# Kernel optimization log

Hardware: AMD Instinct MI355X
Metric: run time of the kernel (lower is better)

The kernel has to match this reference:

```python
import jax, jax.numpy as jnp
import numpy as np

B, S, E, H = 4, 1024, 512, 8
DK = E // H


def setup_inputs() -> dict:
    key = jax.random.key(0)
    ks = jax.random.split(key, 16)
    s = 1.0 / np.sqrt(E)
    inp = {
        "query": jax.random.normal(ks[0], (B, S, E), dtype=jnp.float32),
        "key": jax.random.normal(ks[1], (B, S, E), dtype=jnp.float32),
        "value": jax.random.normal(ks[2], (B, S, E), dtype=jnp.float32),
        "dist_conv": jax.random.uniform(ks[3], (B, S, S), dtype=jnp.float32),
        "mask": jax.random.randint(ks[4], (B, S, S), 0, 2, dtype=jnp.int32),
        # four Linear(E, E) layers: q, k, v, out (torch: y = x @ W.T + b)
        "Wq": jax.random.normal(ks[5], (E, E), dtype=jnp.float32) * s,
        "bq": jnp.zeros((E,), dtype=jnp.float32),
        "Wk": jax.random.normal(ks[6], (E, E), dtype=jnp.float32) * s,
        "bk": jnp.zeros((E,), dtype=jnp.float32),
        "Wv": jax.random.normal(ks[7], (E, E), dtype=jnp.float32) * s,
        "bv": jnp.zeros((E,), dtype=jnp.float32),
        "Wo": jax.random.normal(ks[8], (E, E), dtype=jnp.float32) * s,
        "bo": jnp.zeros((E,), dtype=jnp.float32),
        # 1x1 Conv2d(1, H) -> ReLU -> 1x1 Conv2d(H, H)
        "cw1": jax.random.normal(ks[9], (H,), dtype=jnp.float32),  # [out_c] (in_c=1, k=1)
        "cb1": jnp.zeros((H,), dtype=jnp.float32),
        "cw2": jax.random.normal(ks[10], (H, H), dtype=jnp.float32) * (1.0 / np.sqrt(H)),
        "cb2": jnp.zeros((H,), dtype=jnp.float32),
    }
    return inp


def reference(query, key, value, dist_conv, mask, Wq, bq, Wk, bk, Wv, bv, Wo, bo, cw1, cb1, cw2, cb2):
    # projections, split into heads: [B, H, S, DK]
    def proj(x, W, b):
        y = jnp.einsum("bse,fe->bsf", x, W) + b
        return y.reshape(B, S, H, DK).transpose(0, 2, 1, 3)

    q = proj(query, Wq, bq)
    k = proj(key, Wk, bk)
    v = proj(value, Wv, bv)

    # 1x1 conv stack on distance matrix: [B,S,S] -> [B,H,S,S]
    t = jax.nn.relu(dist_conv[:, None] * cw1[None, :, None, None] + cb1[None, :, None, None])
    bias = jnp.einsum("bhij,gh->bgij", t, cw2) + cb2[None, :, None, None]

    scores = jnp.einsum("bhqd,bhkd->bhqk", q, k) / jnp.sqrt(jnp.float32(DK))
    scores = scores * bias
    scores = jnp.where(mask[:, None] == 0, jnp.float32(-1e9), scores)
    p_attn = jax.nn.softmax(scores, axis=-1)

    x = jnp.einsum("bhqk,bhkd->bhqd", p_attn, v)
    x = x.transpose(0, 2, 1, 3).reshape(B, S, E)
    return jnp.einsum("bse,fe->bsf", x, Wo) + bo
```

## Files before the change

### kernel.cpp

```cpp
#include <hip/hip_runtime.h>
#include <hip/hip_bf16.h>
#include <math.h>

#define B_ 4
#define S_ 1024
#define E_ 512
#define H_ 8
#define DK_ 64

typedef short bf16x8 __attribute__((ext_vector_type(8)));
typedef float f32x4 __attribute__((ext_vector_type(4)));

#define MFMA16(a, b, c) __builtin_amdgcn_mfma_f32_16x16x32_bf16((a), (b), (c), 0, 0, 0)
#define cfence() asm volatile("" ::: "memory")

__device__ __forceinline__ void gl_lds16(const void* gptr, void* lptr) {
    __builtin_amdgcn_global_load_lds(
        (const __attribute__((address_space(1))) unsigned int*)gptr,
        (__attribute__((address_space(3))) unsigned int*)lptr,
        16, 0, 0);
}

__device__ __forceinline__ unsigned short bf16_bits(float v) {
    __hip_bfloat16 h = __float2bfloat16(v);
    return *(unsigned short*)&h;
}

__global__ __launch_bounds__(256) void prep(
    const float* __restrict__ q, const float* __restrict__ k, const float* __restrict__ v,
    const float* __restrict__ wq, const float* __restrict__ wk,
    const float* __restrict__ wv, const float* __restrict__ wo,
    const float* __restrict__ dist, const int* __restrict__ mask,
    const float* __restrict__ cw1, const float* __restrict__ cb1,
    const float* __restrict__ cw2, const float* __restrict__ cb2,
    __hip_bfloat16* qc, __hip_bfloat16* kc, __hip_bfloat16* vc,
    __hip_bfloat16* wqc, __hip_bfloat16* wkc, __hip_bfloat16* wvc, __hip_bfloat16* woc,
    __hip_bfloat16* __restrict__ biasS) {
    const int blk = blockIdx.x;
    if (blk >= 3584) {
        const int bi = blk - 3584;
        const int b = bi >> 10, i = bi & 1023;
        const int j0 = threadIdx.x * 4;
        const size_t dbase = ((size_t)b * 1024 + i) * 1024 + j0;
        float4 d4 = *(const float4*)(dist + dbase);
        int4 m4 = *(const int4*)(mask + dbase);
        float dv[4] = {d4.x, d4.y, d4.z, d4.w};
        int mv[4] = {m4.x, m4.y, m4.z, m4.w};
        float tt[4][8];
#pragma unroll
        for (int e = 0; e < 4; ++e)
#pragma unroll
            for (int h = 0; h < 8; ++h)
                tt[e][h] = fmaxf(fmaf(dv[e], cw1[h], cb1[h]), 0.f);
#pragma unroll
        for (int g = 0; g < 8; ++g) {
            const float c2 = cb2[g];
            union { unsigned short us[4]; uint2 u2; } o;
#pragma unroll
            for (int e = 0; e < 4; ++e) {
                float bv = c2;
#pragma unroll
                for (int h = 0; h < 8; ++h) bv = fmaf(tt[e][h], cw2[g * 8 + h], bv);
                unsigned short u = bf16_bits(bv * 0.125f);
                if (mv[e] == 0) u = 0xFF80u;
                o.us[e] = u;
            }
            *(uint2*)(biasS + ((size_t)(b * 8 + g) * 1024 + i) * 1024 + j0) = o.u2;
        }
        return;
    }
    const float* src;
    __hip_bfloat16* dst;
    int base;
    if (blk < 1024)      { src = q; dst = qc; base = blk; }
    else if (blk < 2048) { src = k; dst = kc; base = blk - 1024; }
    else if (blk < 3072) { src = v; dst = vc; base = blk - 2048; }
    else {
        const int wz = (blk - 3072) >> 7;
        base = (blk - 3072) & 127;
        switch (wz) {
            case 0: src = wq; dst = wqc; break;
            case 1: src = wk; dst = wkc; break;
            case 2: src = wv; dst = wvc; break;
            default: src = wo; dst = woc; break;
        }
    }
    const int idx = (base * 256 + threadIdx.x) * 8;
    float4 a = *(const float4*)(src + idx);
    float4 bb = *(const float4*)(src + idx + 4);
    union { __hip_bfloat16 h[8]; uint4 u; } o;
    o.h[0] = __float2bfloat16(a.x);  o.h[1] = __float2bfloat16(a.y);
    o.h[2] = __float2bfloat16(a.z);  o.h[3] = __float2bfloat16(a.w);
    o.h[4] = __float2bfloat16(bb.x); o.h[5] = __float2bfloat16(bb.y);
    o.h[6] = __float2bfloat16(bb.z); o.h[7] = __float2bfloat16(bb.w);
    *(uint4*)(dst + idx) = o.u;
}

template <int NROWS_W, int NT>
__device__ __forceinline__ void gemm_core128(const __hip_bfloat16* A, const __hip_bfloat16* W,
                                             char* sA, char* sW, int m0, int n0,
                                             f32x4 acc[4][NT]) {
    const int t = threadIdx.x;
    const int w = t >> 6, lane = t & 63;
    const int wm = (w >> 1) * 64, wn = (w & 1) * (NT * 16);
    const int g = lane >> 4, ln = lane & 15;

    for (int kc = 0; kc < 4; ++kc) {
        __syncthreads();
#pragma unroll
        for (int i = 0; i < 8; ++i) {
            int L = (i * 4 + w) * 64 + lane;
            int r = L >> 4, cs = L & 15;
            int c = cs ^ (r & 15);
            gl_lds16((const char*)A + (size_t)(m0 + r) * 1024 + kc * 256 + c * 16,
                     sA + (i * 4 + w) * 1024);
        }
#pragma unroll
        for (int i = 0; i < NROWS_W / 16; ++i) {
            int L = (i * 4 + w) * 64 + lane;
            int r = L >> 4, cs = L & 15;
            int c = cs ^ (r & 15);
            gl_lds16((const char*)W + (size_t)(n0 + r) * 1024 + kc * 256 + c * 16,
                     sW + (i * 4 + w) * 1024);
        }
        __syncthreads();
#pragma unroll
        for (int ks = 0; ks < 4; ++ks) {
            bf16x8 af[4], bf[NT];
#pragma unroll
            for (int mt = 0; mt < 4; ++mt) {
                int m = wm + mt * 16 + ln;
                int c = ks * 4 + g;
                af[mt] = *(const bf16x8*)(sA + m * 256 + (c ^ (m & 15)) * 16);
            }
#pragma unroll
            for (int nt = 0; nt < NT; ++nt) {
                int n = wn + nt * 16 + ln;
                int c = ks * 4 + g;
                bf[nt] = *(const bf16x8*)(sW + n * 256 + (c ^ (n & 15)) * 16);
            }
#pragma unroll
            for (int mt = 0; mt < 4; ++mt)
#pragma unroll
                for (int nt = 0; nt < NT; ++nt)
                    acc[mt][nt] = MFMA16(af[mt], bf[nt], acc[mt][nt]);
        }
    }
}

__global__ __launch_bounds__(256) void proj_gemm(
    const __hip_bfloat16* __restrict__ qc, const __hip_bfloat16* __restrict__ kc,
    const __hip_bfloat16* __restrict__ vc,
    const __hip_bfloat16* __restrict__ wqc, const __hip_bfloat16* __restrict__ wkc,
    const __hip_bfloat16* __restrict__ wvc,
    const float* __restrict__ bq, const float* __restrict__ bk, const float* __restrict__ bv,
    __hip_bfloat16* qbh, __hip_bfloat16* kbh, __hip_bfloat16* vt) {
    __shared__ char smem[65536];
    char* sA = smem;
    char* sW = smem + 32768;
    const int z = blockIdx.z;
    const __hip_bfloat16* A;
    const __hip_bfloat16* W;
    const float* bias;
    __hip_bfloat16* dst;
    if (z == 0)      { A = qc; W = wqc; bias = bq; dst = qbh; }
    else if (z == 1) { A = kc; W = wkc; bias = bk; dst = kbh; }
    else             { A = vc; W = wvc; bias = bv; dst = vt; }

    const int m0 = blockIdx.y * 128, n0 = blockIdx.x * 128;
    f32x4 acc[4][4] = {};
    gemm_core128<128, 4>(A, W, sA, sW, m0, n0, acc);
    __syncthreads();

    const int t = threadIdx.x;
    const int w = t >> 6, lane = t & 63;
    const int wm = (w >> 1) * 64, wn = (w & 1) * 64;
    const int g = lane >> 4, ln = lane & 15;
    const int b = m0 >> 10;
    float bv4[4];
#pragma unroll
    for (int nt = 0; nt < 4; ++nt) bv4[nt] = bias[n0 + wn + nt * 16 + ln];

    __hip_bfloat16* T = (__hip_bfloat16*)smem;
    if (z != 2) {
#pragma unroll
        for (int p = 0; p < 2; ++p) {
            if (wm == p * 64) {
#pragma unroll
                for (int mt = 0; mt < 4; ++mt)
#pragma unroll
                    for (int nt = 0; nt < 4; ++nt)
#pragma unroll
                        for (int r = 0; r < 4; ++r)
                            T[(mt * 16 + g * 4 + r) * 136 + wn + nt * 16 + ln] =
                                __float2bfloat16(acc[mt][nt][r] + bv4[nt]);
            }
            __syncthreads();
            const int lr = t >> 2, quarter = t & 3;
            const char* srow = (const char*)T + lr * 272 + quarter * 64;
            const int s = (m0 & 1023) + p * 64 + lr;
            const int h = (n0 >> 6) + (quarter >> 1);
            char* gdst = (char*)dst +
                         (((size_t)(b * 8 + h) * 1024 + s) * 64 + (quarter & 1) * 32) * 2;
#pragma unroll
            for (int j = 0; j < 4; ++j)
                *(uint4*)(gdst + j * 16) = *(const uint4*)(srow + j * 16);
            __syncthreads();
        }
    } else {
#pragma unroll
        for (int p = 0; p < 2; ++p) {
            if (wm == p * 64) {
#pragma unroll
                for (int mt = 0; mt < 4; ++mt)
#pragma unroll
                    for (int nt = 0; nt < 4; ++nt)
#pragma unroll
                        for (int r = 0; r < 4; ++r)
                            T[(mt * 16 + g * 4 + r) * 130 + wn + nt * 16 + ln] =
                                __float2bfloat16(acc[mt][nt][r] + bv4[nt]);
            }
            __syncthreads();
            const int c = t >> 1, sel = t & 1;
            union { __hip_bfloat16 h[32]; uint4 u[4]; } P;
#pragma unroll
            for (int i = 0; i < 32; ++i)
                P.h[i] = T[(sel * 32 + i) * 130 + c];
            const int h = (n0 >> 6) + (c >> 6), dk = c & 63;
            char* gdst = (char*)vt +
                         (((size_t)(b * 8 + h) * 64 + dk) * 1024 + (m0 & 1023) + p * 64 + sel * 32) * 2;
#pragma unroll
            for (int j = 0; j < 4; ++j)
                *(uint4*)(gdst + j * 16) = P.u[j];
            __syncthreads();
        }
    }
}

__global__ __launch_bounds__(256) void out_gemm(
    const __hip_bfloat16* __restrict__ X, const __hip_bfloat16* __restrict__ woc,
    const float* __restrict__ bo, float* __restrict__ out) {
    __shared__ char smem[49152];
    char* sA = smem;
    char* sW = smem + 32768;
    const int m0 = blockIdx.y * 128, n0 = blockIdx.x * 64;
    f32x4 acc[4][2] = {};
    gemm_core128<64, 2>(X, woc, sA, sW, m0, n0, acc);

    const int t = threadIdx.x;
    const int w = t >> 6, lane = t & 63;
    const int wm = (w >> 1) * 64, wn = (w & 1) * 32;
    const int g = lane >> 4, ln = lane & 15;
    float bv2[2];
#pragma unroll
    for (int nt = 0; nt < 2; ++nt) bv2[nt] = bo[n0 + wn + nt * 16 + ln];
#pragma unroll
    for (int mt = 0; mt < 4; ++mt)
#pragma unroll
        for (int nt = 0; nt < 2; ++nt)
#pragma unroll
            for (int r = 0; r < 4; ++r) {
                int m = m0 + wm + mt * 16 + g * 4 + r;
                int f = n0 + wn + nt * 16 + ln;
                out[(size_t)m * 512 + f] = acc[mt][nt][r] + bv2[nt];
            }
}

__global__ __launch_bounds__(256) void attn_split(
    const __hip_bfloat16* __restrict__ Qb, const __hip_bfloat16* __restrict__ Kb,
    const __hip_bfloat16* __restrict__ Vt, const __hip_bfloat16* __restrict__ biasS,
    float* __restrict__ Op, float2* __restrict__ Ml) {
    __shared__ char sK[8192];
    __shared__ char sV[8192];
    __shared__ char sScP[4][4352];
    __shared__ float sBr[4][16];

    const int t = threadIdx.x, w = t >> 6, lane = t & 63;
    const int g = lane >> 4, ln = lane & 15;
    const int qr = lane >> 2, a = lane & 3;
    const int bh = blockIdx.y;
    const int q0 = blockIdx.x * 64;
    const int spl = blockIdx.z;
    const int kt0 = spl * 512;

    float* sc = (float*)(sScP[w]);
    __hip_bfloat16* sp = (__hip_bfloat16*)(sScP[w]);

    bf16x8 qf[2];
    {
        const char* qbase = (const char*)Qb + ((size_t)bh * 1024 + q0 + w * 16 + ln) * 128;
        qf[0] = *(const bf16x8*)(qbase + g * 16);
        qf[1] = *(const bf16x8*)(qbase + 64 + g * 16);
    }

    const char* kaddr[2];
    const char* vaddr[2];
#pragma unroll
    for (int i = 0; i < 2; ++i) {
        int L = (i * 4 + w) * 64 + lane;
        int r = L >> 3, cs = L & 7;
        int c = cs ^ (r & 7);
        kaddr[i] = (const char*)Kb + (size_t)bh * 131072 + (size_t)(kt0 + r) * 128 + c * 16;
        vaddr[i] = (const char*)Vt + (size_t)bh * 131072 + (size_t)r * 2048 + (size_t)kt0 * 2 + c * 16;
    }
    const char* baddr =
        (const char*)(biasS + ((size_t)bh * 1024 + q0 + w * 16 + qr) * 1024 + kt0 + a * 16);

    float m_st = -1e30f, l_st = 0.f;
    f32x4 O[4] = {};

    for (int it = 0; it < 8; ++it) {
        __syncthreads();
#pragma unroll
        for (int i = 0; i < 2; ++i) {
            gl_lds16(kaddr[i], sK + (i * 4 + w) * 1024);
            gl_lds16(vaddr[i], sV + (i * 4 + w) * 1024);
            kaddr[i] += 8192;
            vaddr[i] += 128;
        }
        union { uint4 u[2]; unsigned short us[16]; } bb;
        bb.u[0] = *(const uint4*)baddr;
        bb.u[1] = *(const uint4*)(baddr + 16);
        baddr += 128;
        __syncthreads();

        f32x4 scv[4] = {};
#pragma unroll
        for (int tt = 0; tt < 4; ++tt)
#pragma unroll
            for (int ks = 0; ks < 2; ++ks) {
                int key = tt * 16 + ln;
                int c = ks * 4 + g;
                bf16x8 kf = *(const bf16x8*)(sK + key * 128 + (c ^ (key & 7)) * 16);
                scv[tt] = MFMA16(qf[ks], kf, scv[tt]);
            }

        cfence();
#pragma unroll
        for (int tt = 0; tt < 4; ++tt)
#pragma unroll
            for (int r = 0; r < 4; ++r)
                sc[(g * 4 + r) * 66 + tt * 16 + ln] = scv[tt][r];
        cfence();

        float sr[16];
        {
            const float* scrow = sc + qr * 66 + a * 16;
#pragma unroll
            for (int j = 0; j < 8; ++j) {
                float2 v2 = *(const float2*)(scrow + j * 2);
                sr[j * 2] = v2.x; sr[j * 2 + 1] = v2.y;
            }
        }
        cfence();

        float mx = -1e30f;
#pragma unroll
        for (int e = 0; e < 16; ++e) {
            unsigned int bits = bb.us[e];
            float f = __uint_as_float(bits << 16);
            float s = sr[e] * f;
            s = (bits == 0xFF80u) ? -1e9f : s;
            sr[e] = s;
            mx = fmaxf(mx, s);
        }
        mx = fmaxf(mx, __shfl_xor(mx, 1));
        mx = fmaxf(mx, __shfl_xor(mx, 2));
        const float mnew = fmaxf(m_st, mx);
        const float alpha = __expf(m_st - mnew);
        m_st = mnew;
        float rs = 0.f;
        union { __hip_bfloat16 hh16[16]; uint4 u[2]; } Pk;
#pragma unroll
        for (int i = 0; i < 16; ++i) {
            float p = __expf(sr[i] - mnew);
            rs += p;
            Pk.hh16[i] = __float2bfloat16(p);
        }
        rs += __shfl_xor(rs, 1);
        rs += __shfl_xor(rs, 2);
        l_st = l_st * alpha + rs;

        *(uint4*)(sp + qr * 72 + a * 16) = Pk.u[0];
        *(uint4*)(sp + qr * 72 + a * 16 + 8) = Pk.u[1];
        cfence();

        if (a == 0) sBr[w][qr] = alpha;
        float al4[4];
#pragma unroll
        for (int r = 0; r < 4; ++r) al4[r] = sBr[w][g * 4 + r];
#pragma unroll
        for (int tt = 0; tt < 4; ++tt)
#pragma unroll
            for (int r = 0; r < 4; ++r) O[tt][r] *= al4[r];

#pragma unroll
        for (int ks = 0; ks < 2; ++ks) {
            bf16x8 pf = *(const bf16x8*)(sp + ln * 72 + ks * 32 + g * 8);
#pragma unroll
            for (int tt = 0; tt < 4; ++tt) {
                int dk = tt * 16 + ln;
                int c = ks * 4 + g;
                bf16x8 vf = *(const bf16x8*)(sV + dk * 128 + (c ^ (dk & 7)) * 16);
                O[tt] = MFMA16(pf, vf, O[tt]);
            }
        }
        cfence();
    }

    const size_t rowbase = ((size_t)spl * 32 + bh) * 1024 + q0 + w * 16;
    if (a == 0) {
        float2 ml2; ml2.x = m_st; ml2.y = l_st;
        Ml[rowbase + qr] = ml2;
    }
#pragma unroll
    for (int r = 0; r < 4; ++r) {
        const int q = g * 4 + r;
#pragma unroll
        for (int tt = 0; tt < 4; ++tt)
            Op[(rowbase + q) * 64 + tt * 16 + ln] = O[tt][r];
    }
}

__global__ __launch_bounds__(256) void combine(
    const float* __restrict__ Op, const float2* __restrict__ Ml,
    __hip_bfloat16* __restrict__ X) {
    const int idx = blockIdx.x * 256 + threadIdx.x;
    const int row = idx >> 5;
    const int pr = (idx & 31) * 2;
    float2 ml1 = Ml[row], ml2 = Ml[32768 + row];
    float m = fmaxf(ml1.x, ml2.x);
    float w1 = __expf(ml1.x - m), w2 = __expf(ml2.x - m);
    float inv = 1.f / fmaf(ml1.y, w1, ml2.y * w2);
    float2 o1 = *(const float2*)(Op + (size_t)row * 64 + pr);
    float2 o2 = *(const float2*)(Op + ((size_t)32768 + row) * 64 + pr);
    float x0 = fmaf(o1.x, w1, o2.x * w2) * inv;
    float x1 = fmaf(o1.y, w1, o2.y * w2) * inv;
    const int bh = row >> 10, s = row & 1023, b = bh >> 3, h = bh & 7;
    union { __hip_bfloat16 hh[2]; unsigned int u; } o;
    o.hh[0] = __float2bfloat16(x0);
    o.hh[1] = __float2bfloat16(x1);
    *(unsigned int*)(X + ((size_t)(b * 1024 + s)) * 512 + h * 64 + pr) = o.u;
}

extern "C" void kernel_launch(void* const* d_in, const int* in_sizes, int n_in,
                              void* d_out, int out_size, void* d_ws, size_t ws_size,
                              hipStream_t stream) {
    (void)in_sizes; (void)n_in; (void)out_size; (void)ws_size;
    const float* query = (const float*)d_in[0];
    const float* key   = (const float*)d_in[1];
    const float* value = (const float*)d_in[2];
    const float* dist  = (const float*)d_in[3];
    const int*   mask  = (const int*)d_in[4];
    const float* Wq = (const float*)d_in[5];
    const float* bq = (const float*)d_in[6];
    const float* Wk = (const float*)d_in[7];
    const float* bk = (const float*)d_in[8];
    const float* Wv = (const float*)d_in[9];
    const float* bv = (const float*)d_in[10];
    const float* Wo = (const float*)d_in[11];
    const float* bo = (const float*)d_in[12];
    const float* cw1 = (const float*)d_in[13];
    const float* cb1 = (const float*)d_in[14];
    const float* cw2 = (const float*)d_in[15];
    const float* cb2 = (const float*)d_in[16];
    float* out = (float*)d_out;

    char* ws = (char*)d_ws;
    const size_t MB = 1 << 20;
    __hip_bfloat16* qc  = (__hip_bfloat16*)(ws + 0 * MB);
    __hip_bfloat16* kc  = (__hip_bfloat16*)(ws + 4 * MB);
    __hip_bfloat16* vc  = (__hip_bfloat16*)(ws + 8 * MB);
    __hip_bfloat16* wqc = (__hip_bfloat16*)(ws + 12 * MB);
    __hip_bfloat16* wkc = (__hip_bfloat16*)(ws + 12 * MB + 512 * 1024);
    __hip_bfloat16* wvc = (__hip_bfloat16*)(ws + 13 * MB);
    __hip_bfloat16* woc = (__hip_bfloat16*)(ws + 13 * MB + 512 * 1024);
    __hip_bfloat16* qbh = (__hip_bfloat16*)(ws + 14 * MB);
    __hip_bfloat16* kbh = (__hip_bfloat16*)(ws + 18 * MB);
    __hip_bfloat16* vt  = (__hip_bfloat16*)(ws + 22 * MB);
    __hip_bfloat16* x   = (__hip_bfloat16*)(ws + 26 * MB);
    __hip_bfloat16* bS  = (__hip_bfloat16*)(ws + 32 * MB);
    float*          Op  = (float*)(ws + 96 * MB);
    float2*         Ml  = (float2*)(ws + 112 * MB);

    hipLaunchKernelGGL(prep, dim3(7680), dim3(256), 0, stream,
                       query, key, value, Wq, Wk, Wv, Wo, dist, mask,
                       cw1, cb1, cw2, cb2,
                       qc, kc, vc, wqc, wkc, wvc, woc, bS);
    hipLaunchKernelGGL(proj_gemm, dim3(4, 32, 3), dim3(256), 0, stream,
                       qc, kc, vc, wqc, wkc, wvc, bq, bk, bv, qbh, kbh, vt);
    hipLaunchKernelGGL(attn_split, dim3(16, 32, 2), dim3(256), 0, stream,
                       qbh, kbh, vt, bS, Op, Ml);
    hipLaunchKernelGGL(combine, dim3(4096), dim3(256), 0, stream, Op, Ml, x);
    hipLaunchKernelGGL(out_gemm, dim3(8, 32), dim3(256), 0, stream,
                       x, woc, bo, out);
}
```

Baseline: 196.1 us.

## Compute conv bias inside attention from packed bf16 dist/mask instead of materialised bias

Prep no longer materialises the per-head bias tensor [B,H,S,S] in bf16. It writes a single [B,S,S] bf16 array that packs the distance and marks masked entries with a negative sentinel. The attention kernel recomputes the two-layer 1x1 conv bias per score in registers, and the 1/sqrt(dk) scale moves into the Q projection. Split-K partial outputs are also stored in bf16 instead of fp32. This cuts global writes and reads of the large bias tensor by roughly 8x, at the cost of extra ALU work in the softmax loop and lower precision in the partial outputs; the sentinel relies on distances being non-negative.

```diff
diff --git a/kernel.cpp b/kernel.cpp
--- a/kernel.cpp
+++ b/kernel.cpp
@@ -31,42 +31,27 @@
     const float* __restrict__ wq, const float* __restrict__ wk,
     const float* __restrict__ wv, const float* __restrict__ wo,
     const float* __restrict__ dist, const int* __restrict__ mask,
-    const float* __restrict__ cw1, const float* __restrict__ cb1,
-    const float* __restrict__ cw2, const float* __restrict__ cb2,
     __hip_bfloat16* qc, __hip_bfloat16* kc, __hip_bfloat16* vc,
     __hip_bfloat16* wqc, __hip_bfloat16* wkc, __hip_bfloat16* wvc, __hip_bfloat16* woc,
-    __hip_bfloat16* __restrict__ biasS) {
+    __hip_bfloat16* __restrict__ md) {
     const int blk = blockIdx.x;
+    const int tid = threadIdx.x;
     if (blk >= 3584) {
-        const int bi = blk - 3584;
-        const int b = bi >> 10, i = bi & 1023;
-        const int j0 = threadIdx.x * 4;
-        const size_t dbase = ((size_t)b * 1024 + i) * 1024 + j0;
-        float4 d4 = *(const float4*)(dist + dbase);
-        int4 m4 = *(const int4*)(mask + dbase);
-        float dv[4] = {d4.x, d4.y, d4.z, d4.w};
-        int mv[4] = {m4.x, m4.y, m4.z, m4.w};
-        float tt[4][8];
-#pragma unroll
-        for (int e = 0; e < 4; ++e)
-#pragma unroll
-            for (int h = 0; h < 8; ++h)
-                tt[e][h] = fmaxf(fmaf(dv[e], cw1[h], cb1[h]), 0.f);
-#pragma unroll
-        for (int g = 0; g < 8; ++g) {
-            const float c2 = cb2[g];
-            union { unsigned short us[4]; uint2 u2; } o;
-#pragma unroll
-            for (int e = 0; e < 4; ++e) {
-                float bv = c2;
-#pragma unroll
-                for (int h = 0; h < 8; ++h) bv = fmaf(tt[e][h], cw2[g * 8 + h], bv);
-                unsigned short u = bf16_bits(bv * 0.125f);
-                if (mv[e] == 0) u = 0xFF80u;
-                o.us[e] = u;
-            }
-            *(uint2*)(biasS + ((size_t)(b * 8 + g) * 1024 + i) * 1024 + j0) = o.u2;
-        }
+        const int idx = ((blk - 3584) * 256 + tid) * 8;
+        float4 d0 = *(const float4*)(dist + idx);
+        float4 d1 = *(const float4*)(dist + idx + 4);
+        int4 m0 = *(const int4*)(mask + idx);
+        int4 m1 = *(const int4*)(mask + idx + 4);
+        union { unsigned short us[8]; uint4 u; } o;
+        o.us[0] = m0.x ? bf16_bits(d0.x) : 0xBF80u;
+        o.us[1] = m0.y ? bf16_bits(d0.y) : 0xBF80u;
+        o.us[2] = m0.z ? bf16_bits(d0.z) : 0xBF80u;
+        o.us[3] = m0.w ? bf16_bits(d0.w) : 0xBF80u;
+        o.us[4] = m1.x ? bf16_bits(d1.x) : 0xBF80u;
+        o.us[5] = m1.y ? bf16_bits(d1.y) : 0xBF80u;
+        o.us[6] = m1.z ? bf16_bits(d1.z) : 0xBF80u;
+        o.us[7] = m1.w ? bf16_bits(d1.w) : 0xBF80u;
+        *(uint4*)(md + idx) = o.u;
         return;
     }
     const float* src;
@@ -85,7 +70,7 @@
             default: src = wo; dst = woc; break;
         }
     }
-    const int idx = (base * 256 + threadIdx.x) * 8;
+    const int idx = (base * 256 + tid) * 8;
     float4 a = *(const float4*)(src + idx);
     float4 bb = *(const float4*)(src + idx + 4);
     union { __hip_bfloat16 h[8]; uint4 u; } o;
@@ -163,9 +148,10 @@
     const __hip_bfloat16* W;
     const float* bias;
     __hip_bfloat16* dst;
-    if (z == 0)      { A = qc; W = wqc; bias = bq; dst = qbh; }
-    else if (z == 1) { A = kc; W = wkc; bias = bk; dst = kbh; }
-    else             { A = vc; W = wvc; bias = bv; dst = vt; }
+    float scale;
+    if (z == 0)      { A = qc; W = wqc; bias = bq; dst = qbh; scale = 0.125f; }
+    else if (z == 1) { A = kc; W = wkc; bias = bk; dst = kbh; scale = 1.f; }
+    else             { A = vc; W = wvc; bias = bv; dst = vt;  scale = 1.f; }
 
     const int m0 = blockIdx.y * 128, n0 = blockIdx.x * 128;
     f32x4 acc[4][4] = {};
@@ -193,7 +179,7 @@
 #pragma unroll
                         for (int r = 0; r < 4; ++r)
                             T[(mt * 16 + g * 4 + r) * 136 + wn + nt * 16 + ln] =
-                                __float2bfloat16(acc[mt][nt][r] + bv4[nt]);
+                                __float2bfloat16((acc[mt][nt][r] + bv4[nt]) * scale);
             }
             __syncthreads();
             const int lr = t >> 2, quarter = t & 3;
@@ -268,8 +254,10 @@
 
 __global__ __launch_bounds__(256) void attn_split(
     const __hip_bfloat16* __restrict__ Qb, const __hip_bfloat16* __restrict__ Kb,
-    const __hip_bfloat16* __restrict__ Vt, const __hip_bfloat16* __restrict__ biasS,
-    float* __restrict__ Op, float2* __restrict__ Ml) {
+    const __hip_bfloat16* __restrict__ Vt, const __hip_bfloat16* __restrict__ md,
+    const float* __restrict__ cw1, const float* __restrict__ cb1,
+    const float* __restrict__ cw2, const float* __restrict__ cb2,
+    __hip_bfloat16* __restrict__ Op, float2* __restrict__ Ml) {
     __shared__ char sK[8192];
     __shared__ char sV[8192];
     __shared__ char sScP[4][4352];
@@ -279,12 +267,20 @@
     const int g = lane >> 4, ln = lane & 15;
     const int qr = lane >> 2, a = lane & 3;
     const int bh = blockIdx.y;
+    const int b = bh >> 3, hblk = bh & 7;
     const int q0 = blockIdx.x * 64;
     const int spl = blockIdx.z;
     const int kt0 = spl * 512;
 
     float* sc = (float*)(sScP[w]);
     __hip_bfloat16* sp = (__hip_bfloat16*)(sScP[w]);
+
+    float w1[8], b1[8], w2[8];
+#pragma unroll
+    for (int i = 0; i < 8; ++i) {
+        w1[i] = cw1[i]; b1[i] = cb1[i]; w2[i] = cw2[hblk * 8 + i];
+    }
+    const float b2v = cb2[hblk];
 
     bf16x8 qf[2];
     {
@@ -303,8 +299,8 @@
         kaddr[i] = (const char*)Kb + (size_t)bh * 131072 + (size_t)(kt0 + r) * 128 + c * 16;
         vaddr[i] = (const char*)Vt + (size_t)bh * 131072 + (size_t)r * 2048 + (size_t)kt0 * 2 + c * 16;
     }
-    const char* baddr =
-        (const char*)(biasS + ((size_t)bh * 1024 + q0 + w * 16 + qr) * 1024 + kt0 + a * 16);
+    const char* mdaddr =
+        (const char*)md + ((size_t)b * 1024 + q0 + w * 16 + qr) * 2048 + (size_t)(kt0 + a * 16) * 2;
 
     float m_st = -1e30f, l_st = 0.f;
     f32x4 O[4] = {};
@@ -319,9 +315,9 @@
             vaddr[i] += 128;
         }
         union { uint4 u[2]; unsigned short us[16]; } bb;
-        bb.u[0] = *(const uint4*)baddr;
-        bb.u[1] = *(const uint4*)(baddr + 16);
-        baddr += 128;
+        bb.u[0] = *(const uint4*)mdaddr;
+        bb.u[1] = *(const uint4*)(mdaddr + 16);
+        mdaddr += 128;
         __syncthreads();
 
         f32x4 scv[4] = {};
@@ -357,10 +353,13 @@
         float mx = -1e30f;
 #pragma unroll
         for (int e = 0; e < 16; ++e) {
-            unsigned int bits = bb.us[e];
-            float f = __uint_as_float(bits << 16);
-            float s = sr[e] * f;
-            s = (bits == 0xFF80u) ? -1e9f : s;
+            float d = __uint_as_float(((unsigned int)bb.us[e]) << 16);
+            float bv = b2v;
+#pragma unroll
+            for (int hh = 0; hh < 8; ++hh)
+                bv = fmaf(fmaxf(fmaf(d, w1[hh], b1[hh]), 0.f), w2[hh], bv);
+            float s = sr[e] * bv;
+            s = (d < 0.f) ? -1e9f : s;
             sr[e] = s;
             mx = fmaxf(mx, s);
         }
@@ -418,12 +417,12 @@
         const int q = g * 4 + r;
 #pragma unroll
         for (int tt = 0; tt < 4; ++tt)
-            Op[(rowbase + q) * 64 + tt * 16 + ln] = O[tt][r];
+            Op[(rowbase + q) * 64 + tt * 16 + ln] = __float2bfloat16(O[tt][r]);
     }
 }
 
 __global__ __launch_bounds__(256) void combine(
-    const float* __restrict__ Op, const float2* __restrict__ Ml,
+    const __hip_bfloat16* __restrict__ Op, const float2* __restrict__ Ml,
     __hip_bfloat16* __restrict__ X) {
     const int idx = blockIdx.x * 256 + threadIdx.x;
     const int row = idx >> 5;
@@ -432,10 +431,12 @@
     float m = fmaxf(ml1.x, ml2.x);
     float w1 = __expf(ml1.x - m), w2 = __expf(ml2.x - m);
     float inv = 1.f / fmaf(ml1.y, w1, ml2.y * w2);
-    float2 o1 = *(const float2*)(Op + (size_t)row * 64 + pr);
-    float2 o2 = *(const float2*)(Op + ((size_t)32768 + row) * 64 + pr);
-    float x0 = fmaf(o1.x, w1, o2.x * w2) * inv;
-    float x1 = fmaf(o1.y, w1, o2.y * w2) * inv;
+    unsigned int u1 = *(const unsigned int*)(Op + (size_t)row * 64 + pr);
+    unsigned int u2 = *(const unsigned int*)(Op + ((size_t)32768 + row) * 64 + pr);
+    float o1x = __uint_as_float(u1 << 16), o1y = __uint_as_float(u1 & 0xFFFF0000u);
+    float o2x = __uint_as_float(u2 << 16), o2y = __uint_as_float(u2 & 0xFFFF0000u);
+    float x0 = fmaf(o1x, w1, o2x * w2) * inv;
+    float x1 = fmaf(o1y, w1, o2y * w2) * inv;
     const int bh = row >> 10, s = row & 1023, b = bh >> 3, h = bh & 7;
     union { __hip_bfloat16 hh[2]; unsigned int u; } o;
     o.hh[0] = __float2bfloat16(x0);
@@ -479,18 +480,17 @@
     __hip_bfloat16* kbh = (__hip_bfloat16*)(ws + 18 * MB);
     __hip_bfloat16* vt  = (__hip_bfloat16*)(ws + 22 * MB);
     __hip_bfloat16* x   = (__hip_bfloat16*)(ws + 26 * MB);
-    __hip_bfloat16* bS  = (__hip_bfloat16*)(ws + 32 * MB);
-    float*          Op  = (float*)(ws + 96 * MB);
-    float2*         Ml  = (float2*)(ws + 112 * MB);
-
-    hipLaunchKernelGGL(prep, dim3(7680), dim3(256), 0, stream,
+    __hip_bfloat16* mdp = (__hip_bfloat16*)(ws + 32 * MB);
+    __hip_bfloat16* Op  = (__hip_bfloat16*)(ws + 48 * MB);
+    float2*         Ml  = (float2*)(ws + 64 * MB);
+
+    hipLaunchKernelGGL(prep, dim3(5632), dim3(256), 0, stream,
                        query, key, value, Wq, Wk, Wv, Wo, dist, mask,
-                       cw1, cb1, cw2, cb2,
-                       qc, kc, vc, wqc, wkc, wvc, woc, bS);
+                       qc, kc, vc, wqc, wkc, wvc, woc, mdp);
     hipLaunchKernelGGL(proj_gemm, dim3(4, 32, 3), dim3(256), 0, stream,
                        qc, kc, vc, wqc, wkc, wvc, bq, bk, bv, qbh, kbh, vt);
     hipLaunchKernelGGL(attn_split, dim3(16, 32, 2), dim3(256), 0, stream,
-                       qbh, kbh, vt, bS, Op, Ml);
+                       qbh, kbh, vt, mdp, cw1, cb1, cw2, cb2, Op, Ml);
     hipLaunchKernelGGL(combine, dim3(4096), dim3(256), 0, stream, Op, Ml, x);
     hipLaunchKernelGGL(out_gemm, dim3(8, 32), dim3(256), 0, stream,
                        x, woc, bo, out);
```

After: 199.5 us. Within noise of the previous version (+1.7%).

## Double-buffer K/V tiles in attention, store partial outputs as bf16, move scale to Q

Applied to the files above, without the earlier changes.

The attention split kernel now double-buffers the K and V shared-memory tiles and prefetches the next bias chunk, so global-to-LDS loads for the next iteration overlap the current iteration's compute. This also removes one barrier per iteration. Partial attention outputs are written as bf16 instead of fp32, halving the write and read traffic between attn_split and combine at some precision cost. The 1/sqrt(dk) scale is folded into the Q projection epilogue instead of the bias tensor, which changes bf16 rounding slightly.

```diff
diff --git a/kernel.cpp b/kernel.cpp
--- a/kernel.cpp
+++ b/kernel.cpp
@@ -37,10 +37,11 @@
     __hip_bfloat16* wqc, __hip_bfloat16* wkc, __hip_bfloat16* wvc, __hip_bfloat16* woc,
     __hip_bfloat16* __restrict__ biasS) {
     const int blk = blockIdx.x;
+    const int tid = threadIdx.x;
     if (blk >= 3584) {
         const int bi = blk - 3584;
         const int b = bi >> 10, i = bi & 1023;
-        const int j0 = threadIdx.x * 4;
+        const int j0 = tid * 4;
         const size_t dbase = ((size_t)b * 1024 + i) * 1024 + j0;
         float4 d4 = *(const float4*)(dist + dbase);
         int4 m4 = *(const int4*)(mask + dbase);
@@ -61,7 +62,7 @@
                 float bv = c2;
 #pragma unroll
                 for (int h = 0; h < 8; ++h) bv = fmaf(tt[e][h], cw2[g * 8 + h], bv);
-                unsigned short u = bf16_bits(bv * 0.125f);
+                unsigned short u = bf16_bits(bv);
                 if (mv[e] == 0) u = 0xFF80u;
                 o.us[e] = u;
             }
@@ -85,7 +86,7 @@
             default: src = wo; dst = woc; break;
         }
     }
-    const int idx = (base * 256 + threadIdx.x) * 8;
+    const int idx = (base * 256 + tid) * 8;
     float4 a = *(const float4*)(src + idx);
     float4 bb = *(const float4*)(src + idx + 4);
     union { __hip_bfloat16 h[8]; uint4 u; } o;
@@ -163,9 +164,10 @@
     const __hip_bfloat16* W;
     const float* bias;
     __hip_bfloat16* dst;
-    if (z == 0)      { A = qc; W = wqc; bias = bq; dst = qbh; }
-    else if (z == 1) { A = kc; W = wkc; bias = bk; dst = kbh; }
-    else             { A = vc; W = wvc; bias = bv; dst = vt; }
+    float scale;
+    if (z == 0)      { A = qc; W = wqc; bias = bq; dst = qbh; scale = 0.125f; }
+    else if (z == 1) { A = kc; W = wkc; bias = bk; dst = kbh; scale = 1.f; }
+    else             { A = vc; W = wvc; bias = bv; dst = vt;  scale = 1.f; }
 
     const int m0 = blockIdx.y * 128, n0 = blockIdx.x * 128;
     f32x4 acc[4][4] = {};
@@ -193,7 +195,7 @@
 #pragma unroll
                         for (int r = 0; r < 4; ++r)
                             T[(mt * 16 + g * 4 + r) * 136 + wn + nt * 16 + ln] =
-                                __float2bfloat16(acc[mt][nt][r] + bv4[nt]);
+                                __float2bfloat16((acc[mt][nt][r] + bv4[nt]) * scale);
             }
             __syncthreads();
             const int lr = t >> 2, quarter = t & 3;
@@ -269,9 +271,9 @@
 __global__ __launch_bounds__(256) void attn_split(
     const __hip_bfloat16* __restrict__ Qb, const __hip_bfloat16* __restrict__ Kb,
     const __hip_bfloat16* __restrict__ Vt, const __hip_bfloat16* __restrict__ biasS,
-    float* __restrict__ Op, float2* __restrict__ Ml) {
-    __shared__ char sK[8192];
-    __shared__ char sV[8192];
+    __hip_bfloat16* __restrict__ Op, float2* __restrict__ Ml) {
+    __shared__ char sK[2][8192];
+    __shared__ char sV[2][8192];
     __shared__ char sScP[4][4352];
     __shared__ float sBr[4][16];
 
@@ -309,20 +311,35 @@
     float m_st = -1e30f, l_st = 0.f;
     f32x4 O[4] = {};
 
+#pragma unroll
+    for (int i = 0; i < 2; ++i) {
+        gl_lds16(kaddr[i], sK[0] + (i * 4 + w) * 1024);
+        gl_lds16(vaddr[i], sV[0] + (i * 4 + w) * 1024);
+        kaddr[i] += 8192;
+        vaddr[i] += 128;
+    }
+    union bbu { uint4 u[2]; unsigned short us[16]; };
+    bbu bb;
+    bb.u[0] = *(const uint4*)baddr;
+    bb.u[1] = *(const uint4*)(baddr + 16);
+    baddr += 128;
+
     for (int it = 0; it < 8; ++it) {
+        const int cur = it & 1;
         __syncthreads();
-#pragma unroll
-        for (int i = 0; i < 2; ++i) {
-            gl_lds16(kaddr[i], sK + (i * 4 + w) * 1024);
-            gl_lds16(vaddr[i], sV + (i * 4 + w) * 1024);
-            kaddr[i] += 8192;
-            vaddr[i] += 128;
-        }
-        union { uint4 u[2]; unsigned short us[16]; } bb;
-        bb.u[0] = *(const uint4*)baddr;
-        bb.u[1] = *(const uint4*)(baddr + 16);
-        baddr += 128;
-        __syncthreads();
+        bbu bbc = bb;
+        if (it < 7) {
+#pragma unroll
+            for (int i = 0; i < 2; ++i) {
+                gl_lds16(kaddr[i], sK[cur ^ 1] + (i * 4 + w) * 1024);
+                gl_lds16(vaddr[i], sV[cur ^ 1] + (i * 4 + w) * 1024);
+                kaddr[i] += 8192;
+                vaddr[i] += 128;
+            }
+            bb.u[0] = *(const uint4*)baddr;
+            bb.u[1] = *(const uint4*)(baddr + 16);
+            baddr += 128;
+        }
 
         f32x4 scv[4] = {};
 #pragma unroll
@@ -331,7 +348,7 @@
             for (int ks = 0; ks < 2; ++ks) {
                 int key = tt * 16 + ln;
                 int c = ks * 4 + g;
-                bf16x8 kf = *(const bf16x8*)(sK + key * 128 + (c ^ (key & 7)) * 16);
+                bf16x8 kf = *(const bf16x8*)(sK[cur] + key * 128 + (c ^ (key & 7)) * 16);
                 scv[tt] = MFMA16(qf[ks], kf, scv[tt]);
             }
 
@@ -357,7 +374,7 @@
         float mx = -1e30f;
 #pragma unroll
         for (int e = 0; e < 16; ++e) {
-            unsigned int bits = bb.us[e];
+            unsigned int bits = bbc.us[e];
             float f = __uint_as_float(bits << 16);
             float s = sr[e] * f;
             s = (bits == 0xFF80u) ? -1e9f : s;
@@ -401,7 +418,7 @@
             for (int tt = 0; tt < 4; ++tt) {
                 int dk = tt * 16 + ln;
                 int c = ks * 4 + g;
-                bf16x8 vf = *(const bf16x8*)(sV + dk * 128 + (c ^ (dk & 7)) * 16);
+                bf16x8 vf = *(const bf16x8*)(sV[cur] + dk * 128 + (c ^ (dk & 7)) * 16);
                 O[tt] = MFMA16(pf, vf, O[tt]);
             }
         }
@@ -418,12 +435,12 @@
         const int q = g * 4 + r;
 #pragma unroll
         for (int tt = 0; tt < 4; ++tt)
-            Op[(rowbase + q) * 64 + tt * 16 + ln] = O[tt][r];
+            Op[(rowbase + q) * 64 + tt * 16 + ln] = __float2bfloat16(O[tt][r]);
     }
 }
 
 __global__ __launch_bounds__(256) void combine(
-    const float* __restrict__ Op, const float2* __restrict__ Ml,
+    const __hip_bfloat16* __restrict__ Op, const float2* __restrict__ Ml,
     __hip_bfloat16* __restrict__ X) {
     const int idx = blockIdx.x * 256 + threadIdx.x;
     const int row = idx >> 5;
@@ -432,10 +449,12 @@
     float m = fmaxf(ml1.x, ml2.x);
     float w1 = __expf(ml1.x - m), w2 = __expf(ml2.x - m);
     float inv = 1.f / fmaf(ml1.y, w1, ml2.y * w2);
-    float2 o1 = *(const float2*)(Op + (size_t)row * 64 + pr);
-    float2 o2 = *(const float2*)(Op + ((size_t)32768 + row) * 64 + pr);
-    float x0 = fmaf(o1.x, w1, o2.x * w2) * inv;
-    float x1 = fmaf(o1.y, w1, o2.y * w2) * inv;
+    unsigned int u1 = *(const unsigned int*)(Op + (size_t)row * 64 + pr);
+    unsigned int u2 = *(const unsigned int*)(Op + ((size_t)32768 + row) * 64 + pr);
+    float o1x = __uint_as_float(u1 << 16), o1y = __uint_as_float(u1 & 0xFFFF0000u);
+    float o2x = __uint_as_float(u2 << 16), o2y = __uint_as_float(u2 & 0xFFFF0000u);
+    float x0 = fmaf(o1x, w1, o2x * w2) * inv;
+    float x1 = fmaf(o1y, w1, o2y * w2) * inv;
     const int bh = row >> 10, s = row & 1023, b = bh >> 3, h = bh & 7;
     union { __hip_bfloat16 hh[2]; unsigned int u; } o;
     o.hh[0] = __float2bfloat16(x0);
@@ -480,7 +499,7 @@
     __hip_bfloat16* vt  = (__hip_bfloat16*)(ws + 22 * MB);
     __hip_bfloat16* x   = (__hip_bfloat16*)(ws + 26 * MB);
     __hip_bfloat16* bS  = (__hip_bfloat16*)(ws + 32 * MB);
-    float*          Op  = (float*)(ws + 96 * MB);
+    __hip_bfloat16* Op  = (__hip_bfloat16*)(ws + 96 * MB);
     float2*         Ml  = (float2*)(ws + 112 * MB);
 
     hipLaunchKernelGGL(prep, dim3(7680), dim3(256), 0, stream,
```

New measurement: 195.8 us. About the same (-0.2%).
